# Performance work log

Measured on AMD Instinct MI355X. Metric: run time of the kernel, lower is better.

Reference implementation:

```python
import jax, jax.numpy as jnp
import numpy as np

D_MODEL = 2048
K_DIM = 128
V_DIM = 128
H = 16
B = 1
S = 2048
SCALE_BASE = 512.0
THETA = 10000.0
EPS = 1e-5


def setup_inputs() -> dict:
    key = jax.random.key(0)
    ks = jax.random.split(key, 11)
    lin = lambda k, i, o: jax.random.normal(k, (i, o), jnp.float32) * 0.02
    return {
        "x": jax.random.normal(ks[0], (B, S, D_MODEL), jnp.float32),
        "Wq": lin(ks[1], D_MODEL, K_DIM * H), "bq": jnp.zeros((K_DIM * H,), jnp.float32),
        "Wk": lin(ks[2], D_MODEL, K_DIM * H), "bk": jnp.zeros((K_DIM * H,), jnp.float32),
        "Wv": lin(ks[3], D_MODEL, V_DIM * H), "bv": jnp.zeros((V_DIM * H,), jnp.float32),
        "Wg": lin(ks[4], D_MODEL, V_DIM * H), "bg": jnp.zeros((V_DIM * H,), jnp.float32),
        "Wo": lin(ks[5], V_DIM * H, D_MODEL), "bo": jnp.zeros((D_MODEL,), jnp.float32),
    }


def _rotate_half(x):
    # interleaved pairs: (x0, x1, x2, x3, ...) -> (-x1, x0, -x3, x2, ...)
    xr = x.reshape(*x.shape[:-1], -1, 2)
    x1, x2 = xr[..., 0], xr[..., 1]
    return jnp.stack((-x2, x1), axis=-1).reshape(x.shape)


def _rope_xpos(q, k, seq_len, dim):
    pos = jnp.arange(seq_len, dtype=jnp.float32)
    inv_freq = 1.0 / (THETA ** (jnp.arange(0, dim, 2, dtype=jnp.float32) / dim))
    freqs = jnp.repeat(pos[:, None] * inv_freq[None, :], 2, axis=-1)  # (S, dim)
    cos, sin = jnp.cos(freqs), jnp.sin(freqs)
    sbase = (jnp.arange(0, dim, 2, dtype=jnp.float32) + 0.4 * dim) / (1.4 * dim)
    power = (pos - seq_len // 2) / SCALE_BASE
    scale = jnp.repeat(sbase[None, :] ** power[:, None], 2, axis=-1)  # (S, dim)
    q = (q * cos + _rotate_half(q) * sin) * scale
    k = (k * cos + _rotate_half(k) * sin) / scale
    return q, k


def reference(x, Wq, bq, Wk, bk, Wv, bv, Wg, bg, Wo, bo):
    Bb, Ss, Dd = x.shape
    heads = lambda t: t.reshape(Bb, Ss, H, -1).transpose(0, 2, 1, 3)  # (B,H,S,d)
    q = heads(x @ Wq + bq)
    k = heads(x @ Wk + bk)
    v = heads(x @ Wv + bv)
    q, k = _rope_xpos(q, k, Ss, K_DIM)
    # per-head decay gamma_h = 1 - 2^{-5-h}
    gamma = 1.0 - 2.0 ** (-5.0 - jnp.arange(H, dtype=jnp.float32))
    pos = jnp.arange(Ss, dtype=jnp.float32)
    pm = pos[:, None] - pos[None, :]  # (S,S)
    decay_mask = jnp.where(pm >= 0, gamma[:, None, None] ** jnp.maximum(pm, 0.0), 0.0)  # (H,S,S)
    scores = jnp.einsum('bhid,bhjd->bhij', q, k) * decay_mask
    ret = jnp.einsum('bhij,bhjd->bhid', scores, v)  # (B,H,S,V_DIM)
    # concat heads and GroupNorm (num_groups=H, affine=False) over flattened rows
    concat = ret.transpose(0, 2, 1, 3).reshape(Bb * Ss, H, V_DIM)
    mu = concat.mean(-1, keepdims=True)
    var = ((concat - mu) ** 2).mean(-1, keepdims=True)
    gn = ((concat - mu) / jnp.sqrt(var + EPS)).reshape(Bb, Ss, H * V_DIM)
    out = (jax.nn.silu(x @ Wg + bg) * gn) @ Wo + bo
    return out
```

## Files before the change

### kernel.cpp

```cpp
#include <hip/hip_runtime.h>
#include <hip/hip_bf16.h>

#define S 2048
#define DM 2048
#define H 16
#define HD 128

using bf16 = __hip_bfloat16;
typedef __attribute__((ext_vector_type(8))) short bf16x8;
typedef __attribute__((ext_vector_type(8))) unsigned short u16x8;
typedef __attribute__((ext_vector_type(4))) float f32x4;

__device__ __forceinline__ unsigned short f2bu(float f) {
  bf16 b = __float2bfloat16(f);
  union { bf16 b; unsigned short u; } cv; cv.b = b; return cv.u;
}
__device__ __forceinline__ float bu2f(unsigned short u) {
  union { bf16 b; unsigned short u; } cv; cv.u = u; return __bfloat162float(cv.b);
}

__device__ __forceinline__ void async_copy16(const void* g, void* l) {
  __builtin_amdgcn_global_load_lds(
      (const __attribute__((address_space(1))) void*)g,
      (__attribute__((address_space(3))) void*)l, 16, 0, 0);
}

__global__ __launch_bounds__(256) void cvt_kernel(const float* __restrict__ x,
                                                  unsigned short* __restrict__ o) {
  int i = (blockIdx.x * 256 + threadIdx.x) * 4;
  float4 v = *(const float4*)(x + i);
  ushort4 r;
  r.x = f2bu(v.x); r.y = f2bu(v.y); r.z = f2bu(v.z); r.w = f2bu(v.w);
  *(ushort4*)(o + i) = r;
}

__global__ __launch_bounds__(256) void wtrans_kernel(
    const float* __restrict__ s0, const float* __restrict__ s1, const float* __restrict__ s2,
    const float* __restrict__ s3, const float* __restrict__ s4,
    unsigned short* __restrict__ d0, unsigned short* __restrict__ d1, unsigned short* __restrict__ d2,
    unsigned short* __restrict__ d3, unsigned short* __restrict__ d4) {
  __shared__ float tile[64][65];
  int z = blockIdx.z;
  const float* src = z == 0 ? s0 : z == 1 ? s1 : z == 2 ? s2 : z == 3 ? s3 : s4;
  unsigned short* dst = z == 0 ? d0 : z == 1 ? d1 : z == 2 ? d2 : z == 3 ? d3 : d4;
  int tid = threadIdx.x;
  int by = blockIdx.y * 64;
  int bx = blockIdx.x * 64;
  int r0 = tid >> 4;
  int c0 = (tid & 15) * 4;
#pragma unroll
  for (int i = 0; i < 4; i++) {
    int row = r0 + i * 16;
    float4 t = *(const float4*)(src + (size_t)(by + row) * DM + bx + c0);
    tile[row][c0 + 0] = t.x; tile[row][c0 + 1] = t.y;
    tile[row][c0 + 2] = t.z; tile[row][c0 + 3] = t.w;
  }
  __syncthreads();
#pragma unroll
  for (int i = 0; i < 4; i++) {
    int nrow = r0 + i * 16;
    ushort4 o;
    o.x = f2bu(tile[c0 + 0][nrow]);
    o.y = f2bu(tile[c0 + 1][nrow]);
    o.z = f2bu(tile[c0 + 2][nrow]);
    o.w = f2bu(tile[c0 + 3][nrow]);
    *(ushort4*)(dst + (size_t)(bx + nrow) * DM + by + c0) = o;
  }
}

__device__ __forceinline__ void stage_half(const unsigned short* gbase, char* ldsbase, int tid) {
#pragma unroll
  for (int r = 0; r < 2; r++) {
    int a = r * 8192 + tid * 16;
    int row = a >> 7;
    int cb = (a & 127) ^ ((row & 7) << 4);
    async_copy16((const unsigned char*)(gbase + (size_t)row * DM) + cb, ldsbase + a);
  }
}

#define LDB4(dst, base, kkofs)                                                                     \
  _Pragma("unroll") for (int nt = 0; nt < 4; ++nt) {                                               \
    int lr = blr0 + nt * 16;                                                                       \
    dst[nt] = *(const bf16x8*)((base) + bhalf + lr * 128 + (((kkofs) + quad * 16) ^ ((lr & 7) << 4))); \
  }
#define LDA4(dst, base, kkofs)                                                                     \
  _Pragma("unroll") for (int mt = 0; mt < 4; ++mt) {                                               \
    int lr = mt * 32 + wm * 16 + r16;                                                              \
    dst[mt] = *(const bf16x8*)((base) + lr * 128 + (((kkofs) + quad * 16) ^ ((lr & 7) << 4)));     \
  }
#define MFMA16(accbase, af, bf)                                                                    \
  _Pragma("unroll") for (int mt = 0; mt < 4; ++mt)                                                 \
    _Pragma("unroll") for (int nt = 0; nt < 4; ++nt)                                               \
      acc[accbase + mt][nt] = __builtin_amdgcn_mfma_f32_16x16x32_bf16(af[mt], bf[nt], acc[accbase + mt][nt], 0, 0, 0);
#define PHASE_SYNC()                                            \
  __builtin_amdgcn_s_barrier();                                 \
  asm volatile("s_waitcnt lgkmcnt(0)" ::: "memory");            \
  __builtin_amdgcn_sched_barrier(0);

__global__ __launch_bounds__(512, 2) void gemm_qkvg_kernel(
    const unsigned short* __restrict__ A, const unsigned short* __restrict__ Bm,
    const float* __restrict__ bias0, const float* __restrict__ bias1,
    const float* __restrict__ bias2, const float* __restrict__ bias3,
    unsigned short* __restrict__ C0, unsigned short* __restrict__ C1,
    unsigned short* __restrict__ Vt, unsigned short* __restrict__ C3) {
  __shared__ alignas(16) char smem[131072];
  char* sA = smem;
  char* sB = smem + 65536;
  int tid = threadIdx.x;
  int wg = blockIdx.y * 32 + blockIdx.x;
  int swz = (wg & 7) * 32 + (wg >> 3);
  int bm = (swz >> 5) * 256;
  int bn = (swz & 31) * 256;
  int wid = tid >> 6, lane = tid & 63;
  int wm = wid >> 2, wn = wid & 3;
  int r16 = lane & 15, quad = lane >> 4;
  f32x4 acc[8][4] = {};
  const int bhalf = (wn >> 1) << 14;
  const int blr0 = ((wn & 1) << 6) + r16;

  stage_half(Bm + (size_t)bn * DM, sB, tid);
  stage_half(Bm + (size_t)(bn + 128) * DM, sB + 16384, tid);
  stage_half(A + (size_t)bm * DM, sA, tid);
  stage_half(A + (size_t)(bm + 128) * DM, sA + 16384, tid);
  stage_half(Bm + (size_t)bn * DM + 64, sB + 32768, tid);
  stage_half(Bm + (size_t)(bn + 128) * DM + 64, sB + 49152, tid);
  asm volatile("s_waitcnt vmcnt(6)" ::: "memory");
  __builtin_amdgcn_s_barrier();

  for (int u = 0; u < 16; ++u) {
    const bool more = u < 15;
    const int k1 = (2 * u + 1) * 64;
    const int k2 = (2 * u + 2) * 64;
    const int k3 = (2 * u + 3) * 64;
    bf16x8 a0[4], a1[4], b0[4], b1[4];

    LDB4(b0, sB, 0)
    LDA4(a0, sA, 0)
    stage_half(A + (size_t)bm * DM + k1, sA + 32768, tid);
    PHASE_SYNC()
    __builtin_amdgcn_s_setprio(1);
    MFMA16(0, a0, b0)
    __builtin_amdgcn_s_setprio(0);

    LDB4(b1, sB, 64)
    LDA4(a1, sA, 64)
    stage_half(A + (size_t)(bm + 128) * DM + k1, sA + 49152, tid);
    asm volatile("s_waitcnt vmcnt(8)" ::: "memory");
    PHASE_SYNC()
    __builtin_amdgcn_s_setprio(1);
    MFMA16(0, a1, b1)
    __builtin_amdgcn_s_setprio(0);

    LDA4(a0, sA + 16384, 0)
    if (more) stage_half(Bm + (size_t)bn * DM + k2, sB, tid);
    PHASE_SYNC()
    __builtin_amdgcn_s_setprio(1);
    MFMA16(4, a0, b0)
    __builtin_amdgcn_s_setprio(0);

    LDA4(a1, sA + 16384, 64)
    if (more) {
      stage_half(Bm + (size_t)(bn + 128) * DM + k2, sB + 16384, tid);
      asm volatile("s_waitcnt vmcnt(6)" ::: "memory");
    } else {
      asm volatile("s_waitcnt vmcnt(2)" ::: "memory");
    }
    PHASE_SYNC()
    __builtin_amdgcn_s_setprio(1);
    MFMA16(4, a1, b1)
    __builtin_amdgcn_s_setprio(0);

    LDB4(b0, sB + 32768, 0)
    LDA4(a0, sA + 32768, 0)
    if (more) stage_half(A + (size_t)bm * DM + k2, sA, tid);
    PHASE_SYNC()
    __builtin_amdgcn_s_setprio(1);
    MFMA16(0, a0, b0)
    __builtin_amdgcn_s_setprio(0);

    LDB4(b1, sB + 32768, 64)
    LDA4(a1, sA + 32768, 64)
    if (more) {
      stage_half(A + (size_t)(bm + 128) * DM + k2, sA + 16384, tid);
      asm volatile("s_waitcnt vmcnt(8)" ::: "memory");
    } else {
      asm volatile("s_waitcnt vmcnt(0)" ::: "memory");
    }
    PHASE_SYNC()
    __builtin_amdgcn_s_setprio(1);
    MFMA16(0, a1, b1)
    __builtin_amdgcn_s_setprio(0);

    LDA4(a0, sA + 32768 + 16384, 0)
    if (more) stage_half(Bm + (size_t)bn * DM + k3, sB + 32768, tid);
    PHASE_SYNC()
    __builtin_amdgcn_s_setprio(1);
    MFMA16(4, a0, b0)
    __builtin_amdgcn_s_setprio(0);

    LDA4(a1, sA + 32768 + 16384, 64)
    if (more) {
      stage_half(Bm + (size_t)(bn + 128) * DM + k3, sB + 49152, tid);
      asm volatile("s_waitcnt vmcnt(6)" ::: "memory");
    }
    PHASE_SYNC()
    __builtin_amdgcn_s_setprio(1);
    MFMA16(4, a1, b1)
    __builtin_amdgcn_s_setprio(0);
  }

  int ch = bn >> 11;
  const float* bp = ch == 0 ? bias0 : ch == 1 ? bias1 : ch == 2 ? bias2 : bias3;
  int lcb = bn & 2047;
  if (ch == 2) {
#pragma unroll
    for (int nt = 0; nt < 4; ++nt) {
      int lc = lcb + wn * 64 + nt * 16 + r16;
      float bv = bp[lc];
#pragma unroll
      for (int mt = 0; mt < 8; ++mt) {
        int m0 = bm + (mt >> 2) * 128 + (mt & 3) * 32 + wm * 16 + quad * 4;
        ushort4 o;
        o.x = f2bu(acc[mt][nt][0] + bv);
        o.y = f2bu(acc[mt][nt][1] + bv);
        o.z = f2bu(acc[mt][nt][2] + bv);
        o.w = f2bu(acc[mt][nt][3] + bv);
        *(ushort4*)(Vt + (size_t)lc * DM + m0) = o;
      }
    }
  } else {
    unsigned short* Cp = ch == 0 ? C0 : ch == 1 ? C1 : C3;
#pragma unroll
    for (int nt = 0; nt < 4; ++nt) {
      int lc = lcb + wn * 64 + nt * 16 + r16;
      float bv = bp[lc];
#pragma unroll
      for (int mt = 0; mt < 8; ++mt) {
        int m0 = bm + (mt >> 2) * 128 + (mt & 3) * 32 + wm * 16 + quad * 4;
#pragma unroll
        for (int rr = 0; rr < 4; ++rr)
          Cp[(size_t)(m0 + rr) * DM + lc] = f2bu(acc[mt][nt][rr] + bv);
      }
    }
  }
}

__device__ __forceinline__ void stage_o(const unsigned short* gA, const unsigned short* gB,
                                        char* dA, char* dB, int tid) {
#pragma unroll
  for (int r = 0; r < 4; r++) {
    int a = r * 4096 + tid * 16;
    int row = a >> 7;
    int cb = (a & 127) ^ ((row & 7) << 4);
    async_copy16((const unsigned char*)(gA + (size_t)row * DM) + cb, dA + a);
  }
#pragma unroll
  for (int r = 0; r < 2; r++) {
    int a = r * 4096 + tid * 16;
    int row = a >> 7;
    int cb = (a & 127) ^ ((row & 7) << 4);
    async_copy16((const unsigned char*)(gB + (size_t)row * DM) + cb, dB + a);
  }
}

__global__ __launch_bounds__(256) void gemm_out_kernel(
    const unsigned short* __restrict__ A, const unsigned short* __restrict__ Bp,
    const float* __restrict__ bias, float* __restrict__ C) {
  __shared__ alignas(16) char sA[2][16384];
  __shared__ alignas(16) char sB[2][8192];
  int tid = threadIdx.x;
  int wg = blockIdx.y * 32 + blockIdx.x;
  int swz = (wg & 7) * 64 + (wg >> 3);
  int bm = (swz >> 5) * 128;
  int bn = (swz & 31) * 64;
  int wid = tid >> 6, lane = tid & 63;
  int wm = wid >> 1, wn = wid & 1;
  int r16 = lane & 15, quad = lane >> 4;
  f32x4 acc[4][2] = {};

  stage_o(A + (size_t)bm * DM, Bp + (size_t)bn * DM, sA[0], sB[0], tid);
  asm volatile("s_waitcnt vmcnt(0)" ::: "memory");
  __builtin_amdgcn_s_barrier();

  for (int t = 0; t < 32; ++t) {
    int cur = t & 1;
    bool more = t < 31;
    int kn = (t + 1) * 64;
    if (more)
      stage_o(A + (size_t)bm * DM + kn, Bp + (size_t)bn * DM + kn, sA[cur ^ 1], sB[cur ^ 1], tid);
#pragma unroll
    for (int kk = 0; kk < 2; kk++) {
      bf16x8 af[4], bfr[2];
#pragma unroll
      for (int mt = 0; mt < 4; mt++) {
        int row = wm * 64 + mt * 16 + r16;
        af[mt] = *(const bf16x8*)(sA[cur] + row * 128 + ((kk * 64 + quad * 16) ^ ((row & 7) << 4)));
      }
#pragma unroll
      for (int nt = 0; nt < 2; nt++) {
        int row = wn * 32 + nt * 16 + r16;
        bfr[nt] = *(const bf16x8*)(sB[cur] + row * 128 + ((kk * 64 + quad * 16) ^ ((row & 7) << 4)));
      }
#pragma unroll
      for (int mt = 0; mt < 4; mt++)
#pragma unroll
        for (int nt = 0; nt < 2; nt++)
          acc[mt][nt] = __builtin_amdgcn_mfma_f32_16x16x32_bf16(af[mt], bfr[nt], acc[mt][nt], 0, 0, 0);
    }
    asm volatile("s_waitcnt vmcnt(0)" ::: "memory");
    __builtin_amdgcn_s_barrier();
  }
#pragma unroll
  for (int nt = 0; nt < 2; nt++) {
    int n = bn + wn * 32 + nt * 16 + r16;
    float bv = bias[n];
#pragma unroll
    for (int mt = 0; mt < 4; mt++) {
      int m0 = bm + wm * 64 + mt * 16 + quad * 4;
#pragma unroll
      for (int r = 0; r < 4; r++)
        C[(size_t)(m0 + r) * DM + n] = acc[mt][nt][r] + bv;
    }
  }
}

__global__ __launch_bounds__(256) void rope_kernel(unsigned short* __restrict__ q,
                                                   unsigned short* __restrict__ k) {
  int idx = blockIdx.x * 256 + threadIdx.x;
  int s = idx >> 10;
  int p = idx & 1023;
  int t = p & 63;
  int head = p >> 6;
  int col = (head << 7) + (t << 1);
  size_t off = (size_t)s * DM + col;
  float ang = (float)s * exp2f((float)(-2 * t) * (13.287712379549449f / 128.0f));
  float sn, cs;
  sincosf(ang, &sn, &cs);
  float sb = ((float)(2 * t) + 51.2f) * (1.0f / 179.2f);
  float power = ((float)s - 1024.0f) * (1.0f / 512.0f);
  float scale = exp2f(power * log2f(sb));
  float l2g = log2f(1.0f - exp2f((float)(-5 - head)));
  float qsc = scale * exp2f((float)s * l2g);
  float ksc = (1.0f / scale) * exp2f(-(float)s * l2g);
  unsigned int qu = *(unsigned int*)(q + off);
  float a = bu2f(qu & 0xffff), b = bu2f(qu >> 16);
  float qa = (a * cs - b * sn) * qsc;
  float qb2 = (b * cs + a * sn) * qsc;
  *(unsigned int*)(q + off) = (unsigned int)f2bu(qa) | ((unsigned int)f2bu(qb2) << 16);
  unsigned int ku = *(unsigned int*)(k + off);
  float c2 = bu2f(ku & 0xffff), d2 = bu2f(ku >> 16);
  float ka = (c2 * cs - d2 * sn) * ksc;
  float kb2 = (d2 * cs + c2 * sn) * ksc;
  *(unsigned int*)(k + off) = (unsigned int)f2bu(ka) | ((unsigned int)f2bu(kb2) << 16);
}

__device__ __forceinline__ void stage_kv(const unsigned short* __restrict__ k,
                                         const unsigned short* __restrict__ vt,
                                         int h, int J0, unsigned char* dK,
                                         unsigned char* dV, int tid) {
#pragma unroll
  for (int r = 0; r < 4; r++) {
    int a = r * 4096 + tid * 16;
    int rowk = a >> 8;
    int cbk = (a & 255) ^ ((rowk & 7) << 4);
    async_copy16((const unsigned char*)(k + (size_t)(J0 + rowk) * DM + h * HD) + cbk, dK + a);
    int rowv = a >> 7;
    int cbv = (a & 127) ^ ((rowv & 7) << 4);
    async_copy16((const unsigned char*)(vt + (size_t)(h * HD + rowv) * DM + J0) + cbv, dV + a);
  }
}

__global__ __launch_bounds__(256) void retention_kernel(
    const unsigned short* __restrict__ q, const unsigned short* __restrict__ k,
    const unsigned short* __restrict__ vt, const unsigned short* __restrict__ g,
    unsigned short* __restrict__ y) {
  __shared__ alignas(16) unsigned char sK[2][16384];
  __shared__ alignas(16) unsigned char sV[2][16384];
  __shared__ alignas(16) unsigned char Plds[8192];
  int bx = blockIdx.x;
  int hi = bx >> 8;
  int h = ((bx >> 5) & 7) | (hi << 3);
  int ib = hi ? (bx & 31) : (31 - (bx & 31));
  int I = ib << 6;
  int tid = threadIdx.x, wid = tid >> 6, lane = tid & 63;
  int r16 = lane & 15, quad = lane >> 4;
  bf16x8 aQ[4];
  size_t qrow = (size_t)(I + wid * 16 + r16);
#pragma unroll
  for (int kk = 0; kk < 4; kk++)
    aQ[kk] = *(const bf16x8*)(q + qrow * DM + h * HD + kk * 32 + quad * 8);
  f32x4 acc[8] = {};
  unsigned char* Pw = Plds + wid * 2048;
  stage_kv(k, vt, h, 0, sK[0], sV[0], tid);
  for (int J0 = 0; J0 <= I; J0 += 64) {
    int cur = (J0 >> 6) & 1;
    bool more = (J0 + 64) <= I;
    if (more) stage_kv(k, vt, h, J0 + 64, sK[cur ^ 1], sV[cur ^ 1], tid);
    if (more) { asm volatile("s_waitcnt vmcnt(8)" ::: "memory"); }
    else      { asm volatile("s_waitcnt vmcnt(0)" ::: "memory"); }
    __builtin_amdgcn_s_barrier();
    const unsigned char* sKc = sK[cur];
    const unsigned char* sVc = sV[cur];
    f32x4 sf[4] = {};
#pragma unroll
    for (int nt = 0; nt < 4; nt++) {
      int row = nt * 16 + r16;
#pragma unroll
      for (int kk = 0; kk < 4; kk++) {
        bf16x8 bK = *(const bf16x8*)(sKc + row * 256 + ((kk * 64 + quad * 16) ^ ((row & 7) << 4)));
        sf[nt] = __builtin_amdgcn_mfma_f32_16x16x32_bf16(aQ[kk], bK, sf[nt], 0, 0, 0);
      }
    }
    bool diag = (J0 == I);
#pragma unroll
    for (int nt = 0; nt < 4; nt++) {
      int j = nt * 16 + r16;
#pragma unroll
      for (int r = 0; r < 4; r++) {
        int ii = wid * 16 + quad * 4 + r;
        float pv = sf[nt][r];
        if (diag && (ii - j) < 0) pv = 0.0f;
        int pr = quad * 4 + r;
        int pcb = (nt * 16 + r16) * 2;
        *(unsigned short*)(Pw + pr * 128 + (pcb ^ ((pr & 7) << 4))) = f2bu(pv);
      }
    }
#pragma unroll
    for (int kk2 = 0; kk2 < 2; kk2++) {
      int cb = kk2 * 64 + quad * 16;
      bf16x8 aP = *(const bf16x8*)(Pw + r16 * 128 + (cb ^ ((r16 & 7) << 4)));
#pragma unroll
      for (int nt2 = 0; nt2 < 8; nt2++) {
        int row = nt2 * 16 + r16;
        bf16x8 bV = *(const bf16x8*)(sVc + row * 128 + ((kk2 * 64 + quad * 16) ^ ((row & 7) << 4)));
        acc[nt2] = __builtin_amdgcn_mfma_f32_16x16x32_bf16(aP, bV, acc[nt2], 0, 0, 0);
      }
    }
    __builtin_amdgcn_s_barrier();
  }
#pragma unroll
  for (int r = 0; r < 4; r++) {
    float sum = 0.0f, sq = 0.0f;
#pragma unroll
    for (int nt2 = 0; nt2 < 8; nt2++) {
      float v = acc[nt2][r];
      sum += v; sq += v * v;
    }
#pragma unroll
    for (int o = 1; o <= 8; o <<= 1) {
      sum += __shfl_xor(sum, o, 64);
      sq += __shfl_xor(sq, o, 64);
    }
    float mean = sum * 0.0078125f;
    float var = sq * 0.0078125f - mean * mean;
    float rstd = rsqrtf(var + 1e-5f);
    int i = I + wid * 16 + quad * 4 + r;
    size_t rowbase = (size_t)i * DM + h * HD;
#pragma unroll
    for (int nt2 = 0; nt2 < 8; nt2++) {
      int col = nt2 * 16 + r16;
      float gv = bu2f(g[rowbase + col]);
      float sg = gv / (1.0f + expf(-gv));
      float yv = sg * (acc[nt2][r] - mean) * rstd;
      y[rowbase + col] = f2bu(yv);
    }
  }
}

extern "C" void kernel_launch(void* const* d_in, const int* in_sizes, int n_in,
                              void* d_out, int out_size, void* d_ws, size_t ws_size,
                              hipStream_t stream) {
  (void)in_sizes; (void)n_in; (void)out_size; (void)ws_size;
  const float* x  = (const float*)d_in[0];
  const float* Wq = (const float*)d_in[1];
  const float* bq = (const float*)d_in[2];
  const float* Wk = (const float*)d_in[3];
  const float* bk = (const float*)d_in[4];
  const float* Wv = (const float*)d_in[5];
  const float* bv = (const float*)d_in[6];
  const float* Wg = (const float*)d_in[7];
  const float* bg = (const float*)d_in[8];
  const float* Wo = (const float*)d_in[9];
  const float* bo = (const float*)d_in[10];

  char* ws = (char*)d_ws;
  const size_t MB = 1ull << 20;
  unsigned short* xb   = (unsigned short*)(ws + 0 * MB);
  unsigned short* wcat = (unsigned short*)(ws + 8 * MB);
  unsigned short* wto  = (unsigned short*)(ws + 40 * MB);
  unsigned short* qb   = (unsigned short*)(ws + 48 * MB);
  unsigned short* kb   = (unsigned short*)(ws + 56 * MB);
  unsigned short* gb   = (unsigned short*)(ws + 72 * MB);
  unsigned short* vt   = (unsigned short*)(ws + 80 * MB);
  unsigned short* yb   = (unsigned short*)(ws + 104 * MB);

  cvt_kernel<<<4096, 256, 0, stream>>>(x, xb);
  wtrans_kernel<<<dim3(32, 32, 5), 256, 0, stream>>>(
      Wq, Wk, Wv, Wg, Wo,
      wcat, wcat + (size_t)2048 * DM, wcat + (size_t)4096 * DM, wcat + (size_t)6144 * DM, wto);
  gemm_qkvg_kernel<<<dim3(32, 8), 512, 0, stream>>>(
      xb, wcat, bq, bk, bv, bg, qb, kb, vt, gb);
  rope_kernel<<<8192, 256, 0, stream>>>(qb, kb);
  retention_kernel<<<512, 256, 0, stream>>>(qb, kb, vt, gb, yb);
  gemm_out_kernel<<<dim3(32, 16), 256, 0, stream>>>(yb, wto, bo, (float*)d_out);
}
```

Before: 171.4 us.

## Fuse RoPE/xPos scaling into QKV GEMM epilogue and x conversion into transpose

Applies the rotary embedding, xPos scale and per-head decay factors directly in the Q/K GEMM epilogue using a lane shuffle to fetch the paired column, removing the standalone rope kernel. The fp32-to-bf16 conversion of x is also folded into the weight transpose launch as an extra grid slice. This removes two kernel launches and a read-modify-write pass over q and k. The epilogue now evaluates transcendentals per element rather than per pair, adding some ALU work to the GEMM.

```diff
diff --git a/kernel.cpp b/kernel.cpp
--- a/kernel.cpp
+++ b/kernel.cpp
@@ -25,29 +25,32 @@
       (__attribute__((address_space(3))) void*)l, 16, 0, 0);
 }
 
-__global__ __launch_bounds__(256) void cvt_kernel(const float* __restrict__ x,
-                                                  unsigned short* __restrict__ o) {
-  int i = (blockIdx.x * 256 + threadIdx.x) * 4;
-  float4 v = *(const float4*)(x + i);
-  ushort4 r;
-  r.x = f2bu(v.x); r.y = f2bu(v.y); r.z = f2bu(v.z); r.w = f2bu(v.w);
-  *(ushort4*)(o + i) = r;
-}
-
 __global__ __launch_bounds__(256) void wtrans_kernel(
     const float* __restrict__ s0, const float* __restrict__ s1, const float* __restrict__ s2,
     const float* __restrict__ s3, const float* __restrict__ s4,
     unsigned short* __restrict__ d0, unsigned short* __restrict__ d1, unsigned short* __restrict__ d2,
-    unsigned short* __restrict__ d3, unsigned short* __restrict__ d4) {
+    unsigned short* __restrict__ d3, unsigned short* __restrict__ d4,
+    const float* __restrict__ x, unsigned short* __restrict__ xb) {
   __shared__ float tile[64][65];
   int z = blockIdx.z;
-  const float* src = z == 0 ? s0 : z == 1 ? s1 : z == 2 ? s2 : z == 3 ? s3 : s4;
-  unsigned short* dst = z == 0 ? d0 : z == 1 ? d1 : z == 2 ? d2 : z == 3 ? d3 : d4;
   int tid = threadIdx.x;
   int by = blockIdx.y * 64;
   int bx = blockIdx.x * 64;
   int r0 = tid >> 4;
   int c0 = (tid & 15) * 4;
+  if (z == 5) {
+#pragma unroll
+    for (int i = 0; i < 4; i++) {
+      int row = by + r0 + i * 16;
+      float4 t = *(const float4*)(x + (size_t)row * DM + bx + c0);
+      ushort4 o;
+      o.x = f2bu(t.x); o.y = f2bu(t.y); o.z = f2bu(t.z); o.w = f2bu(t.w);
+      *(ushort4*)(xb + (size_t)row * DM + bx + c0) = o;
+    }
+    return;
+  }
+  const float* src = z == 0 ? s0 : z == 1 ? s1 : z == 2 ? s2 : z == 3 ? s3 : s4;
+  unsigned short* dst = z == 0 ? d0 : z == 1 ? d1 : z == 2 ? d2 : z == 3 ? d3 : d4;
 #pragma unroll
   for (int i = 0; i < 4; i++) {
     int row = r0 + i * 16;
@@ -228,8 +231,7 @@
         *(ushort4*)(Vt + (size_t)lc * DM + m0) = o;
       }
     }
-  } else {
-    unsigned short* Cp = ch == 0 ? C0 : ch == 1 ? C1 : C3;
+  } else if (ch == 3) {
 #pragma unroll
     for (int nt = 0; nt < 4; ++nt) {
       int lc = lcb + wn * 64 + nt * 16 + r16;
@@ -239,7 +241,39 @@
         int m0 = bm + (mt >> 2) * 128 + (mt & 3) * 32 + wm * 16 + quad * 4;
 #pragma unroll
         for (int rr = 0; rr < 4; ++rr)
-          Cp[(size_t)(m0 + rr) * DM + lc] = f2bu(acc[mt][nt][rr] + bv);
+          C3[(size_t)(m0 + rr) * DM + lc] = f2bu(acc[mt][nt][rr] + bv);
+      }
+    }
+  } else {
+    unsigned short* Cp = ch == 0 ? C0 : C1;
+    float sgn = ch == 0 ? 1.0f : -1.0f;
+#pragma unroll
+    for (int nt = 0; nt < 4; ++nt) {
+      int lc = lcb + wn * 64 + nt * 16 + r16;
+      float bv = bp[lc];
+      int d = lc & 127;
+      int t2 = d & ~1;
+      int head = lc >> 7;
+      float inv = exp2f((float)(-t2) * (13.287712379549449f / 128.0f));
+      float l2sb = log2f(((float)t2 + 51.2f) * (1.0f / 179.2f));
+      float l2g = log2f(1.0f - exp2f((float)(-5 - head)));
+      bool oddd = (d & 1) != 0;
+#pragma unroll
+      for (int mt = 0; mt < 8; ++mt) {
+        int m0 = bm + (mt >> 2) * 128 + (mt & 3) * 32 + wm * 16 + quad * 4;
+#pragma unroll
+        for (int rr = 0; rr < 4; ++rr) {
+          int m = m0 + rr;
+          float v = acc[mt][nt][rr] + bv;
+          float p = __shfl_xor(v, 1, 64);
+          float ang = (float)m * inv;
+          float sn, cs;
+          sincosf(ang, &sn, &cs);
+          float rot = oddd ? (v * cs + p * sn) : (v * cs - p * sn);
+          float e = ((float)m - 1024.0f) * (1.0f / 512.0f) * l2sb + (float)m * l2g;
+          float sc = exp2f(sgn * e);
+          Cp[(size_t)m * DM + lc] = f2bu(rot * sc);
+        }
       }
     }
   }
@@ -322,36 +356,6 @@
         C[(size_t)(m0 + r) * DM + n] = acc[mt][nt][r] + bv;
     }
   }
-}
-
-__global__ __launch_bounds__(256) void rope_kernel(unsigned short* __restrict__ q,
-                                                   unsigned short* __restrict__ k) {
-  int idx = blockIdx.x * 256 + threadIdx.x;
-  int s = idx >> 10;
-  int p = idx & 1023;
-  int t = p & 63;
-  int head = p >> 6;
-  int col = (head << 7) + (t << 1);
-  size_t off = (size_t)s * DM + col;
-  float ang = (float)s * exp2f((float)(-2 * t) * (13.287712379549449f / 128.0f));
-  float sn, cs;
-  sincosf(ang, &sn, &cs);
-  float sb = ((float)(2 * t) + 51.2f) * (1.0f / 179.2f);
-  float power = ((float)s - 1024.0f) * (1.0f / 512.0f);
-  float scale = exp2f(power * log2f(sb));
-  float l2g = log2f(1.0f - exp2f((float)(-5 - head)));
-  float qsc = scale * exp2f((float)s * l2g);
-  float ksc = (1.0f / scale) * exp2f(-(float)s * l2g);
-  unsigned int qu = *(unsigned int*)(q + off);
-  float a = bu2f(qu & 0xffff), b = bu2f(qu >> 16);
-  float qa = (a * cs - b * sn) * qsc;
-  float qb2 = (b * cs + a * sn) * qsc;
-  *(unsigned int*)(q + off) = (unsigned int)f2bu(qa) | ((unsigned int)f2bu(qb2) << 16);
-  unsigned int ku = *(unsigned int*)(k + off);
-  float c2 = bu2f(ku & 0xffff), d2 = bu2f(ku >> 16);
-  float ka = (c2 * cs - d2 * sn) * ksc;
-  float kb2 = (d2 * cs + c2 * sn) * ksc;
-  *(unsigned int*)(k + off) = (unsigned int)f2bu(ka) | ((unsigned int)f2bu(kb2) << 16);
 }
 
 __device__ __forceinline__ void stage_kv(const unsigned short* __restrict__ k,
@@ -494,13 +498,12 @@
   unsigned short* vt   = (unsigned short*)(ws + 80 * MB);
   unsigned short* yb   = (unsigned short*)(ws + 104 * MB);
 
-  cvt_kernel<<<4096, 256, 0, stream>>>(x, xb);
-  wtrans_kernel<<<dim3(32, 32, 5), 256, 0, stream>>>(
+  wtrans_kernel<<<dim3(32, 32, 6), 256, 0, stream>>>(
       Wq, Wk, Wv, Wg, Wo,
-      wcat, wcat + (size_t)2048 * DM, wcat + (size_t)4096 * DM, wcat + (size_t)6144 * DM, wto);
+      wcat, wcat + (size_t)2048 * DM, wcat + (size_t)4096 * DM, wcat + (size_t)6144 * DM, wto,
+      x, xb);
   gemm_qkvg_kernel<<<dim3(32, 8), 512, 0, stream>>>(
       xb, wcat, bq, bk, bv, bg, qb, kb, vt, gb);
-  rope_kernel<<<8192, 256, 0, stream>>>(qb, kb);
   retention_kernel<<<512, 256, 0, stream>>>(qb, kb, vt, gb, yb);
   gemm_out_kernel<<<dim3(32, 16), 256, 0, stream>>>(yb, wto, bo, (float*)d_out);
 }
```

New measurement: 234.0 us. 1.36x slower.
